# Performance work log

Measured on AMD Instinct MI355X. Metric: run time of the kernel, lower is better.

Reference implementation:

```python
import jax, jax.numpy as jnp
import numpy as np

PRIMES = [130003, 130021, 130027, 130043, 130051, 130057, 130069, 130073]
B, S, M, D = 4, 2048, 4, 2048   # batch, seq, hc_mult branches, hidden_size
E, H, DPH = 1024, 8, 128        # total engram embed dim, hash heads, dim per head
K, DIL = 4, 3                    # conv kernel size, dilation (= max ngram size)
EPS_GATE = 1.1920929e-07         # torch RMSNorm default eps (fp32 finfo eps)
EPS_CONV = 1e-5                  # ShortConv norm_eps


def rmsnorm(x, w, eps):
    # x: [..., D], w: broadcastable to [..., D]
    return x * jax.lax.rsqrt(jnp.mean(jnp.square(x), axis=-1, keepdims=True) + eps) * w


def setup_inputs() -> dict:
    key = jax.random.key(0)
    ks = jax.random.split(key, 8)
    total_capacity = int(sum(PRIMES))
    return {
        "hash_indices": jax.random.randint(ks[0], (B, S, H), 0, min(PRIMES)),
        "hidden_states": jax.random.normal(ks[1], (B, S, M, D), jnp.float32),
        "emb_table": jax.random.normal(ks[2], (total_capacity, DPH), jnp.float32) * 0.02,
        "w_v": jax.random.normal(ks[3], (D, E), jnp.float32) * 0.02,      # Linear(E->D) weight [out,in]
        "w_k": jax.random.normal(ks[4], (M, D, E), jnp.float32) * 0.02,   # per-branch Linear(E->D)
        "norm_h_w": jnp.ones((M, D), jnp.float32),
        "norm_k_w": jnp.ones((M, D), jnp.float32),
        "conv_norm_w": jnp.ones((M, D), jnp.float32),
        "conv_w": jax.random.normal(ks[5], (M * D, K), jnp.float32) * 0.02,  # depthwise kernel
    }


def reference(hash_indices, hidden_states, emb_table, w_v, w_k,
              norm_h_w, norm_k_w, conv_norm_w, conv_w):
    # --- multi-head hashed embedding gather (offset into concatenated tables) ---
    offsets = jnp.asarray(np.concatenate([[0], np.cumsum(PRIMES[:-1])]), jnp.int64)
    emb = emb_table[hash_indices + offsets]            # [B,S,H,DPH]
    emb = emb.reshape(B, S, E)                         # flattened engram embedding

    # --- context-aware gating ---
    value = jnp.einsum('bse,de->bsd', emb, w_v)        # [B,S,D]
    keys = jnp.einsum('bse,mde->bsmd', emb, w_k)       # [B,S,M,D]
    nk = rmsnorm(keys, norm_k_w, EPS_GATE)
    nq = rmsnorm(hidden_states, norm_h_w, EPS_GATE)
    score = jnp.sum(nk * nq, axis=-1) / jnp.sqrt(jnp.float32(D))   # [B,S,M]
    g = jnp.sqrt(jnp.maximum(jnp.abs(score), 1e-6)) * jnp.sign(score)
    gate = jax.nn.sigmoid(g)[..., None]                # [B,S,M,1]
    gated = gate * value[:, :, None, :]                # [B,S,M,D]

    # --- ShortConv: SiLU(depthwise causal Conv1d(RMSNorm(gated))) + gated ---
    xn = rmsnorm(gated, conv_norm_w, EPS_CONV)         # per-branch norm, [B,S,M,D]
    xc = xn.transpose(0, 2, 3, 1).reshape(B, M * D, S)  # [B,C,T]
    pad = (K - 1) * DIL
    xp = jnp.pad(xc, ((0, 0), (0, 0), (pad, 0)))
    conv = sum(conv_w[:, k][None, :, None]
               * jax.lax.dynamic_slice_in_dim(xp, k * DIL, S, axis=2)
               for k in range(K))                       # causal depthwise conv
    conv = jax.nn.silu(conv)
    conv = conv.reshape(B, M, D, S).transpose(0, 3, 1, 2)  # [B,S,M,D]
    short_conv_out = conv + gated

    # --- residual to transformer hidden states ---
    return hidden_states + short_conv_out
```

## Files before the change

### kernel.cpp

```cpp
#include <hip/hip_runtime.h>
#include <hip/hip_bf16.h>

#define BDIM 4
#define SDIM 2048
#define MDIM 4
#define DDIM 2048
#define EDIM 1024
#define NTOK 8192
#define NGEMM 10240
#define KDIM 1024
#define NKT 16
#define NPAN 8
#define EPS_GATE 1.1920929e-07f
#define EPS_CONV 1e-5f
#define RSQRT_D 0.022097086912079608f

typedef __bf16 bf16x8 __attribute__((ext_vector_type(8)));
typedef float f32x4 __attribute__((ext_vector_type(4)));
typedef unsigned short ushort8 __attribute__((ext_vector_type(8)));

__constant__ int OFFS[8] = {0, 130003, 260024, 390051, 520094, 650145, 780202, 910271};

__device__ __forceinline__ float bf2f(unsigned short u) {
  union { unsigned int i; float f; } x; x.i = ((unsigned int)u) << 16; return x.f;
}
__device__ __forceinline__ unsigned short f2bf(float f) {
  __hip_bfloat16 h = __float2bfloat16(f);
  unsigned short u; __builtin_memcpy(&u, &h, 2); return u;
}

__global__ __launch_bounds__(256) void k_gather(const int* __restrict__ idx,
                                                const float* __restrict__ table,
                                                unsigned short* __restrict__ embb) {
  const int tok = blockIdx.x;
  const int tid = threadIdx.x;
  const int h = tid >> 5;
  const int e = (tid & 31) * 4;
  const int row = idx[tok * 8 + h] + OFFS[h];
  const float4 v = *(const float4*)(table + (size_t)row * 128 + e);
  ushort4 st;
  st.x = f2bf(v.x); st.y = f2bf(v.y); st.z = f2bf(v.z); st.w = f2bf(v.w);
  *(ushort4*)(embb + (size_t)tok * 1024 + h * 128 + e) = st;
}

__global__ __launch_bounds__(256) void k_cvtw(const float* __restrict__ wv,
                                              const float* __restrict__ wk,
                                              unsigned short* __restrict__ Wb) {
  const size_t i = ((size_t)blockIdx.x * 256 + threadIdx.x) * 4;
  const size_t NV = (size_t)DDIM * EDIM;
  float4 v;
  if (i < NV) v = *(const float4*)(wv + i);
  else        v = *(const float4*)(wk + (i - NV));
  ushort4 st;
  st.x = f2bf(v.x); st.y = f2bf(v.y); st.z = f2bf(v.z); st.w = f2bf(v.w);
  *(ushort4*)(Wb + i) = st;
}

#define GLDS(g, l) __builtin_amdgcn_global_load_lds(                        \
    (const __attribute__((address_space(1))) void*)(g),                    \
    (__attribute__((address_space(3))) void*)(l), 16, 0, 0)

#define BARR() __builtin_amdgcn_s_barrier()
#define LGK0() asm volatile("s_waitcnt lgkmcnt(0)" ::: "memory")
#define VM6()  asm volatile("s_waitcnt vmcnt(6)" ::: "memory")
#define VM0()  asm volatile("s_waitcnt vmcnt(0)" ::: "memory")
#define SB0()  __builtin_amdgcn_sched_barrier(0)

__global__ __launch_bounds__(512, 1) void k_gemm(const unsigned short* __restrict__ A,
                                                 const unsigned short* __restrict__ Bw,
                                                 const float* __restrict__ hidden,
                                                 const float* __restrict__ norm_h,
                                                 const float* __restrict__ norm_k,
                                                 unsigned short* __restrict__ Cv,
                                                 float* __restrict__ skP,
                                                 float* __restrict__ sdP,
                                                 float* __restrict__ shP)
{
  __shared__ __align__(1024) unsigned short lds[65536];
  __shared__ float redk[2][128][4], redd[2][128][4], redh[2][128][4];
  const int tid = threadIdx.x;
  const int lane = tid & 63, wave = tid >> 6;
  const int wm = wave >> 2;
  const int wn = wave & 3;
  const int bid = blockIdx.y * gridDim.x + blockIdx.x;
  const int cpx = (gridDim.x * gridDim.y) >> 3;
  const int swz = (bid & 7) * cpx + (bid >> 3);
  const int row0 = (swz / gridDim.x) * 256;
  const int col0 = (swz % gridDim.x) * 256;
  const int lr = lane & 15;
  const int lg = lane >> 4;

  f32x4 acc[8][4] = {};
  bf16x8 aa[4][2];
  bf16x8 bb[4][2];

#define STG(src, rowbase, kt, gbase)                                           \
  { _Pragma("unroll") for (int l = 0; l < 2; ++l) {                            \
      const int cb = l * 512 + wave * 64;                                      \
      const int chunk = cb + lane;                                             \
      const int rr = chunk >> 3;                                               \
      const int cc = (chunk & 7) ^ (rr & 7);                                   \
      GLDS((src) + (size_t)((rowbase) + rr) * KDIM + (kt) * 64 + cc * 8,       \
           (char*)lds + (gbase) * 2 + cb * 16);                                \
  } }

#define LDA(gbase)                                                             \
  { _Pragma("unroll") for (int a = 0; a < 4; ++a)                              \
    _Pragma("unroll") for (int ks = 0; ks < 2; ++ks)                           \
      aa[a][ks] = *(const bf16x8*)(lds + (gbase) +                             \
          (wm * 64 + a * 16 + lr) * 64 + (((ks * 4 + lg) ^ (lr & 7)) * 8)); }

#define LDB(gbase, n0)                                                         \
  { _Pragma("unroll") for (int n = 0; n < 2; ++n)                              \
    _Pragma("unroll") for (int ks = 0; ks < 2; ++ks)                           \
      bb[(n0) + n][ks] = *(const bf16x8*)(lds + 32768 + (gbase) +              \
          (wn * 32 + n * 16 + lr) * 64 + (((ks * 4 + lg) ^ (lr & 7)) * 8)); }

#define MM(mfb, nfb)                                                           \
  { __builtin_amdgcn_s_setprio(1);                                             \
    _Pragma("unroll") for (int a = 0; a < 4; ++a)                              \
    _Pragma("unroll") for (int n = 0; n < 2; ++n)                              \
    _Pragma("unroll") for (int ks = 0; ks < 2; ++ks)                           \
      acc[(mfb) + a][(nfb) + n] = __builtin_amdgcn_mfma_f32_16x16x32_bf16(     \
          aa[a][ks], bb[(nfb) + n][ks], acc[(mfb) + a][(nfb) + n], 0, 0, 0);   \
    __builtin_amdgcn_s_setprio(0); }

  STG(A,  row0 +   0, 0, 0 * 8192);
  STG(Bw, col0 +   0, 0, 32768 + 0 * 8192);
  STG(Bw, col0 + 128, 0, 32768 + 1 * 8192);
  STG(A,  row0 + 128, 0, 1 * 8192);
  STG(A,  row0 +   0, 1, 2 * 8192);
  STG(Bw, col0 +   0, 1, 32768 + 2 * 8192);
  STG(Bw, col0 + 128, 1, 32768 + 3 * 8192);
  VM6();
  BARR(); SB0();

  for (int kt = 0; kt < NKT; ++kt) {
    const int sA = (kt & 1) * 2;
    const int sN1 = ((kt + 1) & 1) * 2;
    LDA(sA * 8192);
    LDB(sA * 8192, 0);
    if (kt + 1 < NKT) STG(A, row0 + 128, kt + 1, (sN1 + 1) * 8192);
    BARR(); LGK0(); SB0();
    MM(0, 0);
    BARR(); SB0();
    LDB((sA + 1) * 8192, 2);
    if (kt + 2 < NKT) STG(A, row0 + 0, kt + 2, sA * 8192);
    BARR(); LGK0(); SB0();
    MM(0, 2);
    BARR(); SB0();
    LDA((sA + 1) * 8192);
    if (kt + 2 < NKT) STG(Bw, col0 + 0, kt + 2, 32768 + sA * 8192);
    BARR(); LGK0(); SB0();
    MM(4, 2);
    BARR(); SB0();
    if (kt + 2 < NKT) STG(Bw, col0 + 128, kt + 2, 32768 + (sA + 1) * 8192);
    if (kt < NKT - 1) { if (kt == NKT - 2) { VM0(); } else { VM6(); } }
    BARR(); LGK0(); SB0();
    MM(4, 0);
    BARR(); SB0();
  }

  if (col0 < DDIM) {
#pragma unroll
    for (int mf = 0; mf < 8; ++mf) {
#pragma unroll
      for (int nf = 0; nf < 4; ++nf) {
        const int grow = row0 + (mf >> 2) * 128 + wm * 64 + (mf & 3) * 16 + (lane >> 4) * 4;
        const int gcol = col0 + (nf >> 1) * 128 + wn * 32 + (nf & 1) * 16 + lr;
        unsigned short* p = Cv + (size_t)grow * DDIM + gcol;
#pragma unroll
        for (int r = 0; r < 4; ++r) p[(size_t)r * DDIM] = f2bf(acc[mf][nf][r]);
      }
    }
  } else {
    const int m = (col0 - DDIM) >> 11;
    const int dbase = (col0 - DDIM) & (DDIM - 1);
    const int pan = dbase >> 8;
    float* hl = (float*)lds;
    float wkh[4];
#pragma unroll
    for (int nf = 0; nf < 4; ++nf) {
      const int cl = (nf >> 1) * 128 + wn * 32 + (nf & 1) * 16 + lr;
      wkh[nf] = norm_k[m * DDIM + dbase + cl] * norm_h[m * DDIM + dbase + cl];
    }
#pragma unroll
    for (int h = 0; h < 2; ++h) {
      BARR();
#pragma unroll
      for (int i = 0; i < 16; ++i) {
        const int idx = i * 512 + tid;
        const int rl = idx >> 6;
        const int c4 = idx & 63;
        ((float4*)hl)[idx] = *(const float4*)(hidden +
            ((size_t)(row0 + h * 128 + rl) * 4 + m) * DDIM + dbase + c4 * 4);
      }
      BARR();
#pragma unroll
      for (int mf = 0; mf < 4; ++mf) {
#pragma unroll
        for (int r = 0; r < 4; ++r) {
          const int rl = wm * 64 + mf * 16 + (lane >> 4) * 4 + r;
          const int amf = h * 4 + mf;
          float pk = 0.f, pd = 0.f, ph = 0.f;
#pragma unroll
          for (int nf = 0; nf < 4; ++nf) {
            const int cl = (nf >> 1) * 128 + wn * 32 + (nf & 1) * 16 + lr;
            const float kv = acc[amf][nf][r];
            const float hv = hl[rl * 256 + cl];
            pk += kv * kv; ph += hv * hv; pd += kv * hv * wkh[nf];
          }
#pragma unroll
          for (int off = 1; off < 16; off <<= 1) {
            pk += __shfl_xor(pk, off);
            pd += __shfl_xor(pd, off);
            ph += __shfl_xor(ph, off);
          }
          if (lr == 0) {
            redk[h][rl][wn] = pk; redd[h][rl][wn] = pd; redh[h][rl][wn] = ph;
          }
        }
      }
    }
    BARR();
    if (tid < 256) {
      const int h = tid >> 7, rl = tid & 127;
      const int tok = row0 + h * 128 + rl;
      const size_t pidx = ((size_t)tok * 4 + m) * NPAN + pan;
      skP[pidx] = redk[h][rl][0] + redk[h][rl][1] + redk[h][rl][2] + redk[h][rl][3];
      sdP[pidx] = redd[h][rl][0] + redd[h][rl][1] + redd[h][rl][2] + redd[h][rl][3];
      shP[pidx] = redh[h][rl][0] + redh[h][rl][1] + redh[h][rl][2] + redh[h][rl][3];
    }
  }
}

__global__ __launch_bounds__(256) void k_alpha(const unsigned short* __restrict__ valueb,
                                               const float* __restrict__ skP,
                                               const float* __restrict__ sdP,
                                               const float* __restrict__ shP,
                                               float* __restrict__ gates,
                                               float* __restrict__ alphas) {
  const int tok = blockIdx.x;
  const int tid = threadIdx.x, lane = tid & 63, w = tid >> 6;
  __shared__ float red[4];

  float pv = 0.f;
  {
    const ushort8 v8 = *(const ushort8*)(valueb + (size_t)tok * DDIM + tid * 8);
#pragma unroll
    for (int t = 0; t < 8; ++t) { const float f = bf2f(v8[t]); pv += f * f; }
  }
#pragma unroll
  for (int off = 32; off > 0; off >>= 1) pv += __shfl_down(pv, off);
  if (lane == 0) red[w] = pv;
  __syncthreads();

  if (tid < 4) {
    const int m = tid;
    const float msv = (red[0] + red[1] + red[2] + red[3]) * (1.f / 2048.f);
    const size_t base = ((size_t)tok * 4 + m) * NPAN;
    float sk = 0.f, sd = 0.f, sh = 0.f;
#pragma unroll
    for (int q = 0; q < NPAN; ++q) {
      sk += skP[base + q]; sd += sdP[base + q]; sh += shP[base + q];
    }
    const float msk = sk * (1.f / 2048.f) + EPS_GATE;
    const float msh = sh * (1.f / 2048.f) + EPS_GATE;
    const float score = sd * rsqrtf(msk) * rsqrtf(msh) * RSQRT_D;
    const float sgn = (score > 0.f) ? 1.f : ((score < 0.f) ? -1.f : 0.f);
    const float gg = sqrtf(fmaxf(fabsf(score), 1e-6f)) * sgn;
    const float gate = 1.f / (1.f + expf(-gg));
    gates[tok * 4 + m] = gate;
    alphas[tok * 4 + m] = gate * rsqrtf(gate * gate * msv + EPS_CONV);
  }
}

__global__ __launch_bounds__(256) void k_final(const float* __restrict__ hidden,
                                               const unsigned short* __restrict__ valueb,
                                               const float* __restrict__ gates,
                                               const float* __restrict__ alphas,
                                               const float* __restrict__ wcn,
                                               const float* __restrict__ cw,
                                               float* __restrict__ outp) {
  const int lin = blockIdx.x * 256 + threadIdx.x;
  const int d4 = lin & 511;
  const int grp = lin >> 9;
  const int tokbase = grp * 4;
  const int sbase = tokbase & (SDIM - 1);
  const int d = d4 * 4;

  float4 vrow[13];
#pragma unroll
  for (int ri = 0; ri < 13; ++ri) {
    const int off = ri - 9;
    if (sbase + off >= 0) {
      const ushort4 u = *(const ushort4*)(valueb + (size_t)(tokbase + off) * DDIM + d);
      vrow[ri] = make_float4(bf2f(u.x), bf2f(u.y), bf2f(u.z), bf2f(u.w));
    } else vrow[ri] = make_float4(0.f, 0.f, 0.f, 0.f);
  }

#pragma unroll
  for (int m = 0; m < 4; ++m) {
    float cwr[4][4];
#pragma unroll
    for (int i = 0; i < 4; ++i)
      *(float4*)cwr[i] = *(const float4*)(cw + (size_t)(m * DDIM + d + i) * 4);
    const float4 wn = *(const float4*)(wcn + m * DDIM + d);
    float al[13];
#pragma unroll
    for (int ri = 0; ri < 13; ++ri) {
      const int off = ri - 9;
      al[ri] = (sbase + off >= 0) ? alphas[(tokbase + off) * 4 + m] : 0.f;
    }
#pragma unroll
    for (int t = 0; t < 4; ++t) {
      const int tok = tokbase + t;
      const float g = gates[tok * 4 + m];
      const float4 h4 = *(const float4*)(hidden + ((size_t)tok * 4 + m) * DDIM + d);
      float cx = 0.f, cy = 0.f, cz = 0.f, cv = 0.f;
#pragma unroll
      for (int j = 0; j < 4; ++j) {
        const int ri = t + 9 - 3 * j;
        const float aj = al[ri];
        const int tt = 3 - j;
        cx += cwr[0][tt] * aj * vrow[ri].x;
        cy += cwr[1][tt] * aj * vrow[ri].y;
        cz += cwr[2][tt] * aj * vrow[ri].z;
        cv += cwr[3][tt] * aj * vrow[ri].w;
      }
      cx *= wn.x; cy *= wn.y; cz *= wn.z; cv *= wn.w;
      cx = cx / (1.f + expf(-cx));
      cy = cy / (1.f + expf(-cy));
      cz = cz / (1.f + expf(-cz));
      cv = cv / (1.f + expf(-cv));
      const int ri0 = t + 9;
      float4 o;
      o.x = h4.x + g * vrow[ri0].x + cx;
      o.y = h4.y + g * vrow[ri0].y + cy;
      o.z = h4.z + g * vrow[ri0].z + cz;
      o.w = h4.w + g * vrow[ri0].w + cv;
      *(float4*)(outp + ((size_t)tok * 4 + m) * DDIM + d) = o;
    }
  }
}

extern "C" void kernel_launch(void* const* d_in, const int* in_sizes, int n_in,
                              void* d_out, int out_size, void* d_ws, size_t ws_size,
                              hipStream_t stream) {
  const int*   hash_idx = (const int*)d_in[0];
  const float* hidden   = (const float*)d_in[1];
  const float* table    = (const float*)d_in[2];
  const float* w_v      = (const float*)d_in[3];
  const float* w_k      = (const float*)d_in[4];
  const float* norm_h   = (const float*)d_in[5];
  const float* norm_k   = (const float*)d_in[6];
  const float* wcn      = (const float*)d_in[7];
  const float* cw       = (const float*)d_in[8];
  float* outp = (float*)d_out;
  char* ws = (char*)d_ws;

  unsigned short* embb  = (unsigned short*)(ws + 0);
  unsigned short* Wb    = (unsigned short*)(ws + 16777216);
  unsigned short* value = (unsigned short*)(ws + 37748736);
  float*          skP   = (float*)(ws + 71303168);
  float*          sdP   = (float*)(ws + 72351744);
  float*          shP   = (float*)(ws + 73400320);
  float*          gates = (float*)(ws + 74448896);
  float*          alphas= (float*)(ws + 74579968);

  k_gather<<<NTOK, 256, 0, stream>>>(hash_idx, table, embb);
  k_cvtw<<<10240, 256, 0, stream>>>(w_v, w_k, Wb);
  dim3 gg(NGEMM / 256, NTOK / 256);
  k_gemm<<<gg, 512, 0, stream>>>(embb, Wb, hidden, norm_h, norm_k, value, skP, sdP, shP);
  k_alpha<<<NTOK, 256, 0, stream>>>(value, skP, sdP, shP, gates, alphas);
  k_final<<<(NTOK / 4) * 512 / 256, 256, 0, stream>>>(hidden, value, gates, alphas, wcn, cw, outp);
}
```

Before: 420.4 us.

## Merge prep kernels, compute value sum-of-squares in GEMM epilogue, relax final waits

Merges the gather and weight-convert kernels into one launch. Moves the per-token value sum-of-squares into the value-GEMM epilogue as per-panel partials, so k_alpha no longer re-reads the 32 MB bf16 value tensor and becomes a thin one-thread-per-(token,branch) reduction. It also replaces the full vmcnt(0) drain at iteration NKT-2 with staged waits (vmcnt(4), then vmcnt(2)/vmcnt(0) inside the last iteration). The epilogue sums fp32 accumulators rather than rounded bf16 values, so the numerics differ slightly, and it adds a barrier and extra workspace.

```diff
diff --git a/kernel.cpp b/kernel.cpp
--- a/kernel.cpp
+++ b/kernel.cpp
@@ -29,31 +29,33 @@
   unsigned short u; __builtin_memcpy(&u, &h, 2); return u;
 }
 
-__global__ __launch_bounds__(256) void k_gather(const int* __restrict__ idx,
-                                                const float* __restrict__ table,
-                                                unsigned short* __restrict__ embb) {
-  const int tok = blockIdx.x;
+__global__ __launch_bounds__(256) void k_prep(const int* __restrict__ idx,
+                                              const float* __restrict__ table,
+                                              const float* __restrict__ wv,
+                                              const float* __restrict__ wk,
+                                              unsigned short* __restrict__ embb,
+                                              unsigned short* __restrict__ Wb) {
+  const int bid = blockIdx.x;
   const int tid = threadIdx.x;
-  const int h = tid >> 5;
-  const int e = (tid & 31) * 4;
-  const int row = idx[tok * 8 + h] + OFFS[h];
-  const float4 v = *(const float4*)(table + (size_t)row * 128 + e);
-  ushort4 st;
-  st.x = f2bf(v.x); st.y = f2bf(v.y); st.z = f2bf(v.z); st.w = f2bf(v.w);
-  *(ushort4*)(embb + (size_t)tok * 1024 + h * 128 + e) = st;
-}
-
-__global__ __launch_bounds__(256) void k_cvtw(const float* __restrict__ wv,
-                                              const float* __restrict__ wk,
-                                              unsigned short* __restrict__ Wb) {
-  const size_t i = ((size_t)blockIdx.x * 256 + threadIdx.x) * 4;
-  const size_t NV = (size_t)DDIM * EDIM;
-  float4 v;
-  if (i < NV) v = *(const float4*)(wv + i);
-  else        v = *(const float4*)(wk + (i - NV));
-  ushort4 st;
-  st.x = f2bf(v.x); st.y = f2bf(v.y); st.z = f2bf(v.z); st.w = f2bf(v.w);
-  *(ushort4*)(Wb + i) = st;
+  if (bid < NTOK) {
+    const int tok = bid;
+    const int h = tid >> 5;
+    const int e = (tid & 31) * 4;
+    const int row = idx[tok * 8 + h] + OFFS[h];
+    const float4 v = *(const float4*)(table + (size_t)row * 128 + e);
+    ushort4 st;
+    st.x = f2bf(v.x); st.y = f2bf(v.y); st.z = f2bf(v.z); st.w = f2bf(v.w);
+    *(ushort4*)(embb + (size_t)tok * 1024 + h * 128 + e) = st;
+  } else {
+    const size_t i = ((size_t)(bid - NTOK) * 256 + tid) * 4;
+    const size_t NV = (size_t)DDIM * EDIM;
+    float4 v;
+    if (i < NV) v = *(const float4*)(wv + i);
+    else        v = *(const float4*)(wk + (i - NV));
+    ushort4 st;
+    st.x = f2bf(v.x); st.y = f2bf(v.y); st.z = f2bf(v.z); st.w = f2bf(v.w);
+    *(ushort4*)(Wb + i) = st;
+  }
 }
 
 #define GLDS(g, l) __builtin_amdgcn_global_load_lds(                        \
@@ -63,6 +65,8 @@
 #define BARR() __builtin_amdgcn_s_barrier()
 #define LGK0() asm volatile("s_waitcnt lgkmcnt(0)" ::: "memory")
 #define VM6()  asm volatile("s_waitcnt vmcnt(6)" ::: "memory")
+#define VM4()  asm volatile("s_waitcnt vmcnt(4)" ::: "memory")
+#define VM2()  asm volatile("s_waitcnt vmcnt(2)" ::: "memory")
 #define VM0()  asm volatile("s_waitcnt vmcnt(0)" ::: "memory")
 #define SB0()  __builtin_amdgcn_sched_barrier(0)
 
@@ -74,7 +78,8 @@
                                                  unsigned short* __restrict__ Cv,
                                                  float* __restrict__ skP,
                                                  float* __restrict__ sdP,
-                                                 float* __restrict__ shP)
+                                                 float* __restrict__ shP,
+                                                 float* __restrict__ svP)
 {
   __shared__ __align__(1024) unsigned short lds[65536];
   __shared__ float redk[2][128][4], redd[2][128][4], redh[2][128][4];
@@ -141,11 +146,13 @@
     LDA(sA * 8192);
     LDB(sA * 8192, 0);
     if (kt + 1 < NKT) STG(A, row0 + 128, kt + 1, (sN1 + 1) * 8192);
+    if (kt == NKT - 1) { VM2(); }
     BARR(); LGK0(); SB0();
     MM(0, 0);
     BARR(); SB0();
     LDB((sA + 1) * 8192, 2);
     if (kt + 2 < NKT) STG(A, row0 + 0, kt + 2, sA * 8192);
+    if (kt == NKT - 1) { VM0(); }
     BARR(); LGK0(); SB0();
     MM(0, 2);
     BARR(); SB0();
@@ -155,13 +162,15 @@
     MM(4, 2);
     BARR(); SB0();
     if (kt + 2 < NKT) STG(Bw, col0 + 128, kt + 2, 32768 + (sA + 1) * 8192);
-    if (kt < NKT - 1) { if (kt == NKT - 2) { VM0(); } else { VM6(); } }
+    if (kt <= NKT - 3)      { VM6(); }
+    else if (kt == NKT - 2) { VM4(); }
     BARR(); LGK0(); SB0();
     MM(4, 0);
     BARR(); SB0();
   }
 
   if (col0 < DDIM) {
+    const int pan = col0 >> 8;
 #pragma unroll
     for (int mf = 0; mf < 8; ++mf) {
 #pragma unroll
@@ -172,6 +181,32 @@
 #pragma unroll
         for (int r = 0; r < 4; ++r) p[(size_t)r * DDIM] = f2bf(acc[mf][nf][r]);
       }
+    }
+#pragma unroll
+    for (int h = 0; h < 2; ++h) {
+#pragma unroll
+      for (int mf = 0; mf < 4; ++mf) {
+#pragma unroll
+        for (int r = 0; r < 4; ++r) {
+          const int rl = wm * 64 + mf * 16 + (lane >> 4) * 4 + r;
+          const int amf = h * 4 + mf;
+          float pv = 0.f;
+#pragma unroll
+          for (int nf = 0; nf < 4; ++nf) {
+            const float v = acc[amf][nf][r]; pv += v * v;
+          }
+#pragma unroll
+          for (int off = 1; off < 16; off <<= 1) pv += __shfl_xor(pv, off);
+          if (lr == 0) redk[h][rl][wn] = pv;
+        }
+      }
+    }
+    BARR();
+    if (tid < 256) {
+      const int h = tid >> 7, rl = tid & 127;
+      const int tok = row0 + h * 128 + rl;
+      svP[(size_t)tok * NPAN + pan] =
+          redk[h][rl][0] + redk[h][rl][1] + redk[h][rl][2] + redk[h][rl][3];
     }
   } else {
     const int m = (col0 - DDIM) >> 11;
@@ -234,45 +269,30 @@
   }
 }
 
-__global__ __launch_bounds__(256) void k_alpha(const unsigned short* __restrict__ valueb,
-                                               const float* __restrict__ skP,
+__global__ __launch_bounds__(256) void k_alpha(const float* __restrict__ skP,
                                                const float* __restrict__ sdP,
                                                const float* __restrict__ shP,
+                                               const float* __restrict__ svP,
                                                float* __restrict__ gates,
                                                float* __restrict__ alphas) {
-  const int tok = blockIdx.x;
-  const int tid = threadIdx.x, lane = tid & 63, w = tid >> 6;
-  __shared__ float red[4];
-
-  float pv = 0.f;
-  {
-    const ushort8 v8 = *(const ushort8*)(valueb + (size_t)tok * DDIM + tid * 8);
-#pragma unroll
-    for (int t = 0; t < 8; ++t) { const float f = bf2f(v8[t]); pv += f * f; }
-  }
-#pragma unroll
-  for (int off = 32; off > 0; off >>= 1) pv += __shfl_down(pv, off);
-  if (lane == 0) red[w] = pv;
-  __syncthreads();
-
-  if (tid < 4) {
-    const int m = tid;
-    const float msv = (red[0] + red[1] + red[2] + red[3]) * (1.f / 2048.f);
-    const size_t base = ((size_t)tok * 4 + m) * NPAN;
-    float sk = 0.f, sd = 0.f, sh = 0.f;
-#pragma unroll
-    for (int q = 0; q < NPAN; ++q) {
-      sk += skP[base + q]; sd += sdP[base + q]; sh += shP[base + q];
-    }
-    const float msk = sk * (1.f / 2048.f) + EPS_GATE;
-    const float msh = sh * (1.f / 2048.f) + EPS_GATE;
-    const float score = sd * rsqrtf(msk) * rsqrtf(msh) * RSQRT_D;
-    const float sgn = (score > 0.f) ? 1.f : ((score < 0.f) ? -1.f : 0.f);
-    const float gg = sqrtf(fmaxf(fabsf(score), 1e-6f)) * sgn;
-    const float gate = 1.f / (1.f + expf(-gg));
-    gates[tok * 4 + m] = gate;
-    alphas[tok * 4 + m] = gate * rsqrtf(gate * gate * msv + EPS_CONV);
-  }
+  const int idx = blockIdx.x * 256 + threadIdx.x;
+  const int tok = idx >> 2;
+  const size_t base = (size_t)idx * NPAN;
+  float sk = 0.f, sd = 0.f, sh = 0.f, sv = 0.f;
+#pragma unroll
+  for (int q = 0; q < NPAN; ++q) {
+    sk += skP[base + q]; sd += sdP[base + q]; sh += shP[base + q];
+    sv += svP[(size_t)tok * NPAN + q];
+  }
+  const float msv = sv * (1.f / 2048.f);
+  const float msk = sk * (1.f / 2048.f) + EPS_GATE;
+  const float msh = sh * (1.f / 2048.f) + EPS_GATE;
+  const float score = sd * rsqrtf(msk) * rsqrtf(msh) * RSQRT_D;
+  const float sgn = (score > 0.f) ? 1.f : ((score < 0.f) ? -1.f : 0.f);
+  const float gg = sqrtf(fmaxf(fabsf(score), 1e-6f)) * sgn;
+  const float gate = 1.f / (1.f + expf(-gg));
+  gates[idx] = gate;
+  alphas[idx] = gate * rsqrtf(gate * gate * msv + EPS_CONV);
 }
 
 __global__ __launch_bounds__(256) void k_final(const float* __restrict__ hidden,
@@ -365,13 +385,14 @@
   float*          skP   = (float*)(ws + 71303168);
   float*          sdP   = (float*)(ws + 72351744);
   float*          shP   = (float*)(ws + 73400320);
-  float*          gates = (float*)(ws + 74448896);
-  float*          alphas= (float*)(ws + 74579968);
-
-  k_gather<<<NTOK, 256, 0, stream>>>(hash_idx, table, embb);
-  k_cvtw<<<10240, 256, 0, stream>>>(w_v, w_k, Wb);
+  float*          svP   = (float*)(ws + 74448896);
+  float*          gates = (float*)(ws + 74711040);
+  float*          alphas= (float*)(ws + 74842112);
+
+  k_prep<<<NTOK + 10240, 256, 0, stream>>>(hash_idx, table, w_v, w_k, embb, Wb);
   dim3 gg(NGEMM / 256, NTOK / 256);
-  k_gemm<<<gg, 512, 0, stream>>>(embb, Wb, hidden, norm_h, norm_k, value, skP, sdP, shP);
-  k_alpha<<<NTOK, 256, 0, stream>>>(value, skP, sdP, shP, gates, alphas);
+  k_gemm<<<gg, 512, 0, stream>>>(embb, Wb, hidden, norm_h, norm_k, value,
+                                 skP, sdP, shP, svP);
+  k_alpha<<<NTOK * MDIM / 256, 256, 0, stream>>>(skP, sdP, shP, svP, gates, alphas);
   k_final<<<(NTOK / 4) * 512 / 256, 256, 0, stream>>>(hidden, value, gates, alphas, wcn, cw, outp);
 }
```

Measured after the change: 417.7 us (median of 2 runs). Within noise of the previous version (-0.7%).
